# Performance work log

Measured on AMD Instinct MI355X. Metric: run time of the kernel, lower is better.

The kernel has to match this reference:

```python
import jax, jax.numpy as jnp
import numpy as np

C = 1024
HEADS = 8
HEAD_DIM = C // HEADS
SCALE = HEAD_DIM ** -0.5
GROUPS = 32
EPS = 1e-5


def _conv3(x, w, b):
    # 3x3x3 conv, padding=1 (SAME), NCDHW
    y = jax.lax.conv_general_dilated(x, w, (1, 1, 1), 'SAME',
                                     dimension_numbers=('NCDHW', 'OIDHW', 'NCDHW'))
    return y + b[None, :, None, None, None]


def _proj(x, w, b):
    # 1x1x1 conv == channel matmul; w: (C_out, C_in)
    return jnp.einsum('oc,bcdhw->bodhw', w, x) + b[None, :, None, None, None]


def _gn(x, g, b):
    B, Ch, D, H, W = x.shape
    xr = x.reshape(B, GROUPS, Ch // GROUPS, D, H, W)
    mu = xr.mean(axis=(2, 3, 4, 5), keepdims=True)
    var = xr.var(axis=(2, 3, 4, 5), keepdims=True)
    xn = ((xr - mu) * jax.lax.rsqrt(var + EPS)).reshape(B, Ch, D, H, W)
    return xn * g[None, :, None, None, None] + b[None, :, None, None, None]


def _attn(q, k, v):
    # q,k,v: (B,C,D,H,W) -> heads over channels, tokens over flattened spatial
    B, Ch, D, H, W = q.shape
    S = D * H * W
    q = q.reshape(B, HEADS, HEAD_DIM, S)
    k = k.reshape(B, HEADS, HEAD_DIM, S)
    v = v.reshape(B, HEADS, HEAD_DIM, S)
    logits = jnp.einsum('bhds,bhdt->bhst', q, k) * SCALE  # (B,H,S,S)
    a = jax.nn.softmax(logits, axis=-1)
    o = jnp.einsum('bhst,bhdt->bhds', a, v)
    return o.reshape(B, Ch, D, H, W)


def setup_inputs() -> dict:
    key = jax.random.key(0)
    ks = iter(jax.random.split(key, 40))
    def w(shape, s=0.02):
        return jax.random.normal(next(ks), shape, dtype=jnp.float32) * s
    B, D, H, W = 2, 8, 16, 16
    inp = {'x': jax.random.normal(next(ks), (B, C, D, H, W), dtype=jnp.float32)}
    for side in ('l', 'r'):
        inp[f'conv_{side}_w'] = w((C, C, 3, 3, 3))
        inp[f'conv_{side}_b'] = jnp.zeros((C,), jnp.float32)
        inp[f'gn_{side}_g'] = jnp.ones((C,), jnp.float32)
        inp[f'gn_{side}_b'] = jnp.zeros((C,), jnp.float32)
    for name in ('ql', 'kr', 'vr', 'qr', 'kl', 'vl'):
        inp[f'{name}_w'] = w((C, C))
        inp[f'{name}_b'] = jnp.zeros((C,), jnp.float32)
    inp['fus_w'] = w((C, C))
    inp['fus_b'] = jnp.zeros((C,), jnp.float32)
    inp['gn_f_g'] = jnp.ones((C,), jnp.float32)
    inp['gn_f_b'] = jnp.zeros((C,), jnp.float32)
    return inp


def reference(x, conv_l_w, conv_l_b, gn_l_g, gn_l_b,
              conv_r_w, conv_r_b, gn_r_g, gn_r_b,
              ql_w, ql_b, kr_w, kr_b, vr_w, vr_b,
              qr_w, qr_b, kl_w, kl_b, vl_w, vl_b,
              fus_w, fus_b, gn_f_g, gn_f_b):
    W = x.shape[-1]
    mid = W // 2
    x_left = x[..., :mid]
    x_right = x[..., mid:2 * mid]
    f_l = jax.nn.relu(_gn(_conv3(x_left, conv_l_w, conv_l_b), gn_l_g, gn_l_b))
    f_r = jax.nn.relu(_gn(_conv3(x_right, conv_r_w, conv_r_b), gn_r_g, gn_r_b))
    rf = jnp.flip(f_r, axis=-1)
    # left attends to flipped right
    out_l = _attn(_proj(f_l, ql_w, ql_b), _proj(rf, kr_w, kr_b), _proj(rf, vr_w, vr_b))
    # flipped right attends to left
    out_r = _attn(_proj(rf, qr_w, qr_b), _proj(f_l, kl_w, kl_b), _proj(f_l, vl_w, vl_b))
    asym_map = jnp.abs(f_l - rf).mean(axis=1, keepdims=True)
    out_r = jnp.flip(out_r, axis=-1)
    f_concat = jnp.concatenate([out_l, out_r], axis=-1)  # W even -> no pad needed
    fused = jax.nn.relu(_gn(_proj(f_concat, fus_w, fus_b), gn_f_g, gn_f_b))
    return fused, asym_map
```

## Files before the change

### kernel.cpp

```cpp
#include <hip/hip_runtime.h>
#include <hip/hip_bf16.h>
#include <stdint.h>


using bf16_t = __bf16;
using bf16x4 = __attribute__((ext_vector_type(4))) __bf16;
using bf16x8 = __attribute__((ext_vector_type(8))) __bf16;
using f32x4  = __attribute__((ext_vector_type(4))) float;

typedef const uint32_t __attribute__((address_space(1)))* gas1_t;
typedef uint32_t __attribute__((address_space(3)))* las3_t;

__device__ __forceinline__ f32x4 mfma16(bf16x8 a, bf16x8 b, f32x4 c) {
  return __builtin_amdgcn_mfma_f32_16x16x32_bf16(a, b, c, 0, 0, 0);
}
__device__ __forceinline__ void gload_lds16(const void* g, void* l) {
  __builtin_amdgcn_global_load_lds((gas1_t)g, (las3_t)l, 16, 0, 0);
}

__global__ __launch_bounds__(256) void convw_kernel(
    const float* __restrict__ wl, const float* __restrict__ wr,
    bf16_t* __restrict__ Wb)
{
  const int chunk = blockIdx.x;
  const int co    = blockIdx.y;
  const int side  = blockIdx.z;
  const float* __restrict__ src = (side ? wr : wl) + (size_t)co * 27648 + (size_t)chunk * 6912;
  __shared__ float L[6912];
  __shared__ bf16_t Lb[27][260];
  const int tid = threadIdx.x;
  for (int i = tid; i < 1728; i += 256)
    *(float4*)&L[i << 2] = *(const float4*)&src[i << 2];
  __syncthreads();
  {
    const int ci = tid;
#pragma unroll
    for (int t = 0; t < 27; ++t)
      Lb[t][ci] = (bf16_t)L[ci * 27 + t];
  }
  __syncthreads();
  bf16_t* __restrict__ dst = Wb + (size_t)side * (1024u * 27648u) + (size_t)co * 27648 + (chunk << 8);
  for (int u = tid; u < 864; u += 256) {
    const int t = u >> 5, c8 = (u & 31) << 3;
    const bf16x8 v = *(const bf16x8*)&Lb[t][c8];
    *(bf16x8*)&dst[(t << 10) + c8] = v;
  }
}

__global__ __launch_bounds__(256) void projw_kernel(
    const float* ql, const float* kl, const float* kr, const float* qr,
    const float* vl, const float* vr, const float* fu,
    bf16_t* __restrict__ Wp, float qs)
{
  const int z = blockIdx.y;
  const float* src; float s = 1.f;
  switch (z) {
    case 0: src = ql; s = qs; break;
    case 1: src = kl; break;
    case 2: src = kr; break;
    case 3: src = qr; s = qs; break;
    case 4: src = vl; break;
    case 5: src = vr; break;
    default: src = fu; break;
  }
  const size_t i4 = ((size_t)blockIdx.x * 256 + threadIdx.x) * 4;
  const float4 v = *(const float4*)(src + i4);
  bf16x4 o;
  o[0] = (bf16_t)(v.x * s); o[1] = (bf16_t)(v.y * s);
  o[2] = (bf16_t)(v.z * s); o[3] = (bf16_t)(v.w * s);
  *(bf16x4*)(Wp + (size_t)z * 1048576 + i4) = o;
}

__global__ __launch_bounds__(256) void xp_build_kernel(
    const float* __restrict__ x, bf16_t* __restrict__ Xp)
{
  const int cc0  = blockIdx.x << 6;
  const int d    = blockIdx.y;
  const int sb   = blockIdx.z;
  const int side = sb >> 1, b = sb & 1;
  __shared__ bf16_t Tls[64][132];
  const int tid = threadIdx.x;
#pragma unroll
  for (int j = 0; j < 8; ++j) {
    const int u = tid + (j << 8);
    const int ci = u >> 5, sub = u & 31;
    const int hh = sub >> 1, half = sub & 1;
    const float4 v = *(const float4*)&x[((size_t)((b << 10) + cc0 + ci) * 8 + d) * 256 +
                                        (hh << 4) + (side << 3) + (half << 2)];
    bf16x4 o;
    o[0] = (bf16_t)v.x; o[1] = (bf16_t)v.y; o[2] = (bf16_t)v.z; o[3] = (bf16_t)v.w;
    *(bf16x4*)&Tls[ci][(hh << 3) + (half << 2)] = o;
  }
  __syncthreads();
  bf16_t* __restrict__ dst = Xp + (size_t)side * 3686400 + (size_t)b * 1843200;
#pragma unroll
  for (int j = 0; j < 4; ++j) {
    const int u = tid + (j << 8);
    const int hw = u >> 3, c8 = u & 7;
    const int hh = hw >> 3, ww = hw & 7;
    bf16x8 v;
#pragma unroll
    for (int e = 0; e < 8; ++e) v[e] = Tls[(c8 << 3) + e][hw];
    *(bf16x8*)&dst[(size_t)(((d + 1) * 18 + (hh + 1)) * 10 + (ww + 1)) * 1024 + cc0 + (c8 << 3)] = v;
  }
}

__global__ __launch_bounds__(256, 4) void conv_gemm_kernel(
    const bf16_t* __restrict__ Wb, const bf16_t* __restrict__ Xp,
    bf16_t* __restrict__ Pb)
{
  const int bid = blockIdx.x;
  const int orig = ((bid & 7) << 7) | (bid >> 3);
  const int n     = orig & 15;
  const int m0    = ((orig >> 4) & 7) << 7;
  const int side  = (orig >> 7) & 1;
  const int slice = orig >> 8;
  const int t0 = slice * 7;
  const int t1 = (slice == 3) ? 27 : t0 + 7;
  const int b = n >> 3, d = n & 7;

  const bf16_t* __restrict__ A = Wb + (size_t)side * (1024u * 27648u);
  const bf16_t* __restrict__ X = Xp + (size_t)side * 3686400 + (size_t)b * 1843200;

  __shared__ bf16_t Asm[128 * 64];
  __shared__ bf16_t Bsm[128 * 64];

  const int tid = threadIdx.x;
  const int lane = tid & 63;
  const int wv = tid >> 6;
  const int wm = wv >> 1, wn = wv & 1;
  const int lane15 = lane & 15, lane4 = lane >> 4;
  const int srow0 = (wv << 5) + (lane >> 3);
  const int sc = lane & 7;

  const f32x4 fz = {0.f, 0.f, 0.f, 0.f};
  f32x4 acc[4][4];
#pragma unroll
  for (int i = 0; i < 4; ++i)
#pragma unroll
    for (int j = 0; j < 4; ++j) acc[i][j] = fz;

  for (int t = t0; t < t1; ++t) {
    const int kd = t / 9, kh = (t / 3) % 3, kw = t % 3;
    const int sb0 = ((d + kd) * 18 + kh) * 10 + kw;
    for (int cb = 0; cb < 16; ++cb) {
      const int kofs = (t << 10) + (cb << 6);
#pragma unroll
      for (int i = 0; i < 4; ++i) {
        const int row = srow0 + (i << 3);
        gload_lds16(A + (size_t)(m0 + row) * 27648 + kofs + ((sc ^ (row & 7)) << 3),
                    &Asm[((wv << 2) + i) << 9]);
      }
#pragma unroll
      for (int i = 0; i < 4; ++i) {
        const int row = srow0 + (i << 3);
        const int hh = row >> 3, ww = row & 7;
        gload_lds16(X + (size_t)(sb0 + hh * 10 + ww) * 1024 + (cb << 6) + ((sc ^ (row & 7)) << 3),
                    &Bsm[((wv << 2) + i) << 9]);
      }
      __syncthreads();
#pragma unroll
      for (int ks = 0; ks < 2; ++ks) {
        bf16x8 af[4];
#pragma unroll
        for (int mi = 0; mi < 4; ++mi) {
          const int row = (wm << 6) + (mi << 4) + lane15;
          const int ch = ((ks << 2) + lane4) ^ (row & 7);
          af[mi] = *(const bf16x8*)&Asm[(row << 6) + (ch << 3)];
        }
#pragma unroll
        for (int ni = 0; ni < 4; ++ni) {
          const int row = (wn << 6) + (ni << 4) + lane15;
          const int ch = ((ks << 2) + lane4) ^ (row & 7);
          const bf16x8 bfr = *(const bf16x8*)&Bsm[(row << 6) + (ch << 3)];
#pragma unroll
          for (int mi = 0; mi < 4; ++mi)
            acc[mi][ni] = mfma16(af[mi], bfr, acc[mi][ni]);
        }
      }
      __syncthreads();
    }
  }

  bf16_t* __restrict__ P = Pb + (((size_t)(slice << 1) + side) << 21);
  const int colbase = (b << 10) + (d << 7) + (wn << 6);
#pragma unroll
  for (int mi = 0; mi < 4; ++mi) {
    const int row0 = m0 + (wm << 6) + (mi << 4) + (lane4 << 2);
#pragma unroll
    for (int r = 0; r < 4; ++r) {
#pragma unroll
      for (int ni = 0; ni < 4; ++ni) {
        const int col = colbase + (ni << 4) + lane15;
        P[((size_t)(row0 + r) << 11) + col] = (bf16_t)acc[mi][ni][r];
      }
    }
  }
}

__global__ __launch_bounds__(256) void reduce4_kernel(
    const bf16_t* __restrict__ Pb, const float* __restrict__ bias_l,
    const float* __restrict__ bias_r, bf16_t* __restrict__ out_l, bf16_t* __restrict__ out_r,
    float* __restrict__ pS_lr, float* __restrict__ pQ_lr)
{
  const int id = blockIdx.x * 256 + threadIdx.x;
  const int tid = threadIdx.x;
  const int c8 = id & 255;
  const int co = (id >> 8) & 1023;
  const int side = id >> 18;
  const size_t off = ((size_t)co << 11) + ((size_t)c8 << 3);
  const float bia = (side ? bias_r : bias_l)[co];
  float acc[8];
#pragma unroll
  for (int e = 0; e < 8; ++e) acc[e] = bia;
#pragma unroll
  for (int s = 0; s < 4; ++s) {
    const bf16x8 v = *(const bf16x8*)&Pb[(((size_t)(s << 1) + side) << 21) + off];
#pragma unroll
    for (int e = 0; e < 8; ++e) acc[e] += (float)v[e];
  }
  bf16x8 ov;
#pragma unroll
  for (int e = 0; e < 8; ++e) ov[e] = (bf16_t)acc[e];
  *(bf16x8*)((side ? out_r : out_l) + off) = ov;
  float s = 0.f, q = 0.f;
#pragma unroll
  for (int e = 0; e < 8; ++e) { s += acc[e]; q += acc[e] * acc[e]; }
  __shared__ float sb[8];
  const int lane = tid & 63, wv = tid >> 6;
#pragma unroll
  for (int o = 1; o < 64; o <<= 1) { s += __shfl_xor(s, o, 64); q += __shfl_xor(q, o, 64); }
  if (lane == 0) { sb[wv] = s; sb[4 + wv] = q; }
  __syncthreads();
  if (tid == 0) {
    const int g = (side << 6) + (co >> 5);
    atomicAdd(&pS_lr[g],      sb[0] + sb[1]);
    atomicAdd(&pS_lr[g + 32], sb[2] + sb[3]);
    atomicAdd(&pQ_lr[g],      sb[4] + sb[5]);
    atomicAdd(&pQ_lr[g + 32], sb[6] + sb[7]);
  }
}

__device__ __forceinline__ void gemm_accum(
    const bf16_t* __restrict__ A, int lda,
    const bf16_t* __restrict__ Bt, int ldb,
    int K, f32x4 acc[4][4])
{
  __shared__ bf16_t Asm[128 * 64];
  __shared__ bf16_t Bsm[128 * 64];
  const int tid = threadIdx.x;
  const int lane = tid & 63;
  const int wv = tid >> 6;
  const int wm = wv >> 1, wn = wv & 1;
  const int lane15 = lane & 15, lane4 = lane >> 4;
  const int srow0 = (wv << 5) + (lane >> 3);
  const int sc = lane & 7;

  for (int k0 = 0; k0 < K; k0 += 64) {
#pragma unroll
    for (int i = 0; i < 4; ++i) {
      const int row = srow0 + (i << 3);
      gload_lds16(A + (size_t)row * lda + k0 + ((sc ^ (row & 7)) << 3),
                  &Asm[((wv << 2) + i) << 9]);
    }
#pragma unroll
    for (int i = 0; i < 4; ++i) {
      const int row = srow0 + (i << 3);
      gload_lds16(Bt + (size_t)row * ldb + k0 + ((sc ^ (row & 7)) << 3),
                  &Bsm[((wv << 2) + i) << 9]);
    }
    __syncthreads();
#pragma unroll
    for (int ks = 0; ks < 2; ++ks) {
      bf16x8 af[4];
#pragma unroll
      for (int mi = 0; mi < 4; ++mi) {
        const int row = (wm << 6) + (mi << 4) + lane15;
        const int ch = ((ks << 2) + lane4) ^ (row & 7);
        af[mi] = *(const bf16x8*)&Asm[(row << 6) + (ch << 3)];
      }
#pragma unroll
      for (int ni = 0; ni < 4; ++ni) {
        const int row = (wn << 6) + (ni << 4) + lane15;
        const int ch = ((ks << 2) + lane4) ^ (row & 7);
        const bf16x8 bfr = *(const bf16x8*)&Bsm[(row << 6) + (ch << 3)];
#pragma unroll
        for (int mi = 0; mi < 4; ++mi)
          acc[mi][ni] = mfma16(af[mi], bfr, acc[mi][ni]);
      }
    }
    __syncthreads();
  }
}

struct ProjTArgs {
  const bf16_t* act[2];
  const float*  bias[2][2];
  float         scl[2][2];
  bf16_t*       outp[2][2];
};
__global__ __launch_bounds__(256) void proj_t_kernel(const bf16_t* __restrict__ Wp, ProjTArgs a)
{
  const int side = blockIdx.z;
  const int n0 = blockIdx.x << 7;
  const int m0 = blockIdx.y << 7;
  const int seg = m0 >> 10;
  const f32x4 fz = {0.f, 0.f, 0.f, 0.f};
  f32x4 acc[4][4];
#pragma unroll
  for (int i = 0; i < 4; ++i)
#pragma unroll
    for (int j = 0; j < 4; ++j) acc[i][j] = fz;
  gemm_accum(a.act[side] + (size_t)n0 * 1024, 1024,
             Wp + (size_t)side * 2097152 + (size_t)m0 * 1024, 1024, 1024, acc);

  const int lane = threadIdx.x & 63, wv = threadIdx.x >> 6;
  const int wm = wv >> 1, wn = wv & 1;
  const int lane15 = lane & 15, lane4 = lane >> 4;
  const float* __restrict__ bias = a.bias[side][seg];
  const float bscale = a.scl[side][seg];
  bf16_t* __restrict__ C = a.outp[side][seg];
  const int mloc = (m0 & 1023) + (wn << 6);
  float bv[4];
#pragma unroll
  for (int ni = 0; ni < 4; ++ni) bv[ni] = bias[mloc + (ni << 4) + lane15] * bscale;
#pragma unroll
  for (int mi = 0; mi < 4; ++mi) {
    const int rowb = n0 + (wm << 6) + (mi << 4) + (lane4 << 2);
#pragma unroll
    for (int r = 0; r < 4; ++r) {
#pragma unroll
      for (int ni = 0; ni < 4; ++ni) {
        const int col = mloc + (ni << 4) + lane15;
        C[(size_t)(rowb + r) * 1024 + col] = (bf16_t)(acc[mi][ni][r] + bv[ni]);
      }
    }
  }
}

__global__ __launch_bounds__(256) void proj_v_kernel(
    const bf16_t* __restrict__ Wp, const bf16_t* __restrict__ flT,
    const bf16_t* __restrict__ rfT, const float* __restrict__ vlb,
    const float* __restrict__ vrb, bf16_t* __restrict__ Vl, bf16_t* __restrict__ Vr)
{
  const int side = blockIdx.z;
  const int m0 = blockIdx.x << 7;
  const int n0 = blockIdx.y << 7;
  const f32x4 fz = {0.f, 0.f, 0.f, 0.f};
  f32x4 acc[4][4];
#pragma unroll
  for (int i = 0; i < 4; ++i)
#pragma unroll
    for (int j = 0; j < 4; ++j) acc[i][j] = fz;
  gemm_accum(Wp + 4194304ull + (size_t)side * 1048576 + (size_t)m0 * 1024, 1024,
             (side ? rfT : flT) + (size_t)n0 * 1024, 1024, 1024, acc);

  const int lane = threadIdx.x & 63, wv = threadIdx.x >> 6;
  const int wm = wv >> 1, wn = wv & 1;
  const int lane15 = lane & 15, lane4 = lane >> 4;
  const float* __restrict__ bias = side ? vrb : vlb;
  bf16_t* __restrict__ C = side ? Vr : Vl;
#pragma unroll
  for (int mi = 0; mi < 4; ++mi) {
    const int row0 = m0 + (wm << 6) + (mi << 4) + (lane4 << 2);
#pragma unroll
    for (int r = 0; r < 4; ++r) {
      const float bia = bias[row0 + r];
#pragma unroll
      for (int ni = 0; ni < 4; ++ni) {
        const int col = n0 + (wn << 6) + (ni << 4) + lane15;
        C[(size_t)(row0 + r) * 2048 + col] = (bf16_t)(acc[mi][ni][r] + bia);
      }
    }
  }
}

__global__ __launch_bounds__(256) void fused_gemm_kernel(
    const bf16_t* __restrict__ Wf, const bf16_t* __restrict__ Bt, bf16_t* __restrict__ Pf)
{
  const int z = blockIdx.z;
  const int m0 = blockIdx.x << 7;
  const int n0 = blockIdx.y << 7;
  const f32x4 fz = {0.f, 0.f, 0.f, 0.f};
  f32x4 acc[4][4];
#pragma unroll
  for (int i = 0; i < 4; ++i)
#pragma unroll
    for (int j = 0; j < 4; ++j) acc[i][j] = fz;
  gemm_accum(Wf + (size_t)m0 * 1024 + (z << 9), 1024,
             Bt + (size_t)n0 * 1024 + (z << 9), 1024, 512, acc);

  const int lane = threadIdx.x & 63, wv = threadIdx.x >> 6;
  const int wm = wv >> 1, wn = wv & 1;
  const int lane15 = lane & 15, lane4 = lane >> 4;
  bf16_t* __restrict__ C = Pf + ((size_t)z << 22);
#pragma unroll
  for (int mi = 0; mi < 4; ++mi) {
    const int row0 = m0 + (wm << 6) + (mi << 4) + (lane4 << 2);
#pragma unroll
    for (int r = 0; r < 4; ++r) {
#pragma unroll
      for (int ni = 0; ni < 4; ++ni) {
        const int col = n0 + (wn << 6) + (ni << 4) + lane15;
        C[(size_t)(row0 + r) * 4096 + col] = (bf16_t)acc[mi][ni][r];
      }
    }
  }
}

__global__ __launch_bounds__(256) void gn_apply_lr_kernel(
    const bf16_t* __restrict__ yl, const bf16_t* __restrict__ yr,
    const float* __restrict__ gl, const float* __restrict__ bl,
    const float* __restrict__ gr, const float* __restrict__ br,
    const float* __restrict__ pS_lr, const float* __restrict__ pQ_lr,
    bf16_t* __restrict__ flT, bf16_t* __restrict__ rfT)
{
  const int side = blockIdx.z;
  const int n0 = blockIdx.x << 6;
  const int c0 = blockIdx.y << 6;
  const bf16_t* __restrict__ y = side ? yr : yl;
  const float* __restrict__ gamma = side ? gr : gl;
  const float* __restrict__ beta  = side ? br : bl;
  __shared__ float L[64][65];
  const int tid = threadIdx.x;
#pragma unroll
  for (int j = 0; j < 2; ++j) {
    const int u = tid + (j << 8);
    const int cr = u >> 3, ch = u & 7;
    const bf16x8 v = *(const bf16x8*)&y[(size_t)(c0 + cr) * 2048 + n0 + (ch << 3)];
#pragma unroll
    for (int e = 0; e < 8; ++e) L[cr][(ch << 3) + e] = (float)v[e];
  }
  __syncthreads();
  const int b = n0 >> 10;
  bf16_t* __restrict__ outT = side ? rfT : flT;
#pragma unroll
  for (int j = 0; j < 2; ++j) {
    const int u = tid + (j << 8);
    const int nr = u >> 3, c8 = u & 7;
    const int n = n0 + nr;
    const int nf = side ? ((n & ~7) | (7 - (n & 7))) : n;
    const int cbase = c0 + (c8 << 3);
    const int gidx = (side << 6) + (b << 5) + (cbase >> 5);
    const float m = pS_lr[gidx] * (1.f / 32768.f);
    const float rs = rsqrtf(pQ_lr[gidx] * (1.f / 32768.f) - m * m + 1e-5f);
    bf16x8 v;
#pragma unroll
    for (int e = 0; e < 8; ++e) {
      const int c = cbase + e;
      const float xv = (L[(c8 << 3) + e][nr] - m) * rs * gamma[c] + beta[c];
      v[e] = (bf16_t)fmaxf(xv, 0.f);
    }
    *(bf16x8*)&outT[(size_t)nf * 1024 + cbase] = v;
  }
}

__global__ __launch_bounds__(256, 2) void attn_kernel(
    const bf16_t* __restrict__ qlt, const bf16_t* __restrict__ krt, const bf16_t* __restrict__ vrm,
    const bf16_t* __restrict__ qrt, const bf16_t* __restrict__ klt, const bf16_t* __restrict__ vlm,
    bf16_t* __restrict__ xfc)
{
  const int st = blockIdx.x;
  const int bh = blockIdx.y;
  const int az = blockIdx.z;
  const int b = bh >> 3, h = bh & 7;
  const bf16_t* __restrict__ qt = az ? qrt : qlt;
  const bf16_t* __restrict__ kt = az ? klt : krt;
  const bf16_t* __restrict__ vm = az ? vlm : vrm;

  __shared__ bf16_t Ks[64 * 128];
  __shared__ bf16_t Vs[128 * 64];
  __shared__ bf16_t Ps[4][16 * 64];

  const int tid = threadIdx.x, lane = tid & 63, wv = tid >> 6;
  const int lane15 = lane & 15, lane4 = lane >> 4;

  bf16x8 qf[4];
  {
    const bf16_t* __restrict__ qbase = qt + (size_t)((b << 10) + (st << 6)) * 1024 + (h << 7);
    const int row = (wv << 4) + lane15;
#pragma unroll
    for (int kk = 0; kk < 4; ++kk)
      qf[kk] = *(const bf16x8*)&qbase[(size_t)row * 1024 + (kk << 5) + (lane4 << 3)];
  }

  const f32x4 fz = {0.f, 0.f, 0.f, 0.f};
  f32x4 oacc[8];
#pragma unroll
  for (int nj = 0; nj < 8; ++nj) oacc[nj] = fz;
  float mrun[4], lrun[4];
#pragma unroll
  for (int r = 0; r < 4; ++r) { mrun[r] = -3.0e38f; lrun[r] = 0.f; }

  for (int it = 0; it < 16; ++it) {
    __syncthreads();
#pragma unroll
    for (int j = 0; j < 4; ++j) {
      const int g = (wv << 2) + j;
      const int row = (g << 2) + lane4;
      gload_lds16(kt + (size_t)((b << 10) + (it << 6) + row) * 1024 + (h << 7) + ((lane15 ^ (row & 7)) << 3),
                  &Ks[g << 9]);
    }
#pragma unroll
    for (int j = 0; j < 4; ++j) {
      const int g = (wv << 2) + j;
      const int row = (g << 3) + (lane >> 3);
      gload_lds16(vm + (size_t)((h << 7) + row) * 2048 + (b << 10) + (it << 6) + (((lane & 7) ^ (row & 7)) << 3),
                  &Vs[g << 9]);
    }
    __syncthreads();
    f32x4 la[4];
#pragma unroll
    for (int tj = 0; tj < 4; ++tj) la[tj] = fz;
#pragma unroll
    for (int kk = 0; kk < 4; ++kk) {
#pragma unroll
      for (int tj = 0; tj < 4; ++tj) {
        const int row = (tj << 4) + lane15;
        const int ch = ((kk << 2) + lane4) ^ (row & 7);
        const bf16x8 kf = *(const bf16x8*)&Ks[(row << 7) + (ch << 3)];
        la[tj] = mfma16(qf[kk], kf, la[tj]);
      }
    }
    float mx[4];
    int ok = 1;
#pragma unroll
    for (int r = 0; r < 4; ++r) {
      float m_ = la[0][r];
#pragma unroll
      for (int tj = 1; tj < 4; ++tj) m_ = fmaxf(m_, la[tj][r]);
#pragma unroll
      for (int o = 1; o < 16; o <<= 1) m_ = fmaxf(m_, __shfl_xor(m_, o, 64));
      mx[r] = m_;
      ok &= (m_ <= mrun[r] + 8.f) ? 1 : 0;
    }
    if (!__all(ok)) {
#pragma unroll
      for (int r = 0; r < 4; ++r) {
        const float mnew = fmaxf(mrun[r], mx[r]);
        const float alpha = __builtin_amdgcn_exp2f(mrun[r] - mnew);
        mrun[r] = mnew;
        lrun[r] *= alpha;
#pragma unroll
        for (int nj = 0; nj < 8; ++nj) oacc[nj][r] *= alpha;
      }
    }
#pragma unroll
    for (int r = 0; r < 4; ++r) {
      const int row = (lane4 << 2) + r;
      float rs = 0.f;
#pragma unroll
      for (int tj = 0; tj < 4; ++tj) {
        const float p = __builtin_amdgcn_exp2f(la[tj][r] - mrun[r]);
        rs += p;
        const int byte_ = ((tj << 5) + (lane15 << 1)) ^ ((row & 7) << 4);
        *(bf16_t*)((char*)(&Ps[wv][0]) + (row << 7) + byte_) = (bf16_t)p;
      }
#pragma unroll
      for (int o = 1; o < 16; o <<= 1) rs += __shfl_xor(rs, o, 64);
      lrun[r] += rs;
    }
#pragma unroll
    for (int kk = 0; kk < 2; ++kk) {
      const int prow = lane15;
      const int pch = ((kk << 2) + lane4) ^ (prow & 7);
      const bf16x8 pf = *(const bf16x8*)&Ps[wv][(prow << 6) + (pch << 3)];
#pragma unroll
      for (int nj = 0; nj < 8; ++nj) {
        const int row = (nj << 4) + lane15;
        const int ch = ((kk << 2) + lane4) ^ (row & 7);
        const bf16x8 vf = *(const bf16x8*)&Vs[(row << 6) + (ch << 3)];
        oacc[nj] = mfma16(pf, vf, oacc[nj]);
      }
    }
  }
#pragma unroll
  for (int r = 0; r < 4; ++r) {
    const int sl = (wv << 4) + (lane4 << 2) + r;
    const int s = (st << 6) + sl;
    const int dd = s >> 7, hh2 = (s >> 3) & 15, ww = s & 7;
    const int w16 = az ? (15 - ww) : ww;
    const int n16 = (b << 11) + ((dd << 4) + hh2) * 16 + w16;
    const float inv = 1.f / lrun[r];
#pragma unroll
    for (int nj = 0; nj < 8; ++nj) {
      const int c = (h << 7) + (nj << 4) + lane15;
      xfc[(size_t)n16 * 1024 + c] = (bf16_t)(oacc[nj][r] * inv);
    }
  }
}

__global__ __launch_bounds__(256) void gn_partial_f_kernel(
    const bf16_t* __restrict__ Pf, const float* __restrict__ bias,
    float* __restrict__ pS, float* __restrict__ pQ)
{
  const int bg = blockIdx.x;
  const int sl = blockIdx.y;
  const int b = bg >> 5, g = bg & 31;
  const int tid = threadIdx.x;
  const int c = (g << 5) + (tid >> 3);
  const int s0 = (sl << 8) + ((tid & 7) << 5);
  const size_t base = (size_t)c * 4096 + (b << 11) + s0;
  const float bia = bias[c];
  float s = 0.f, q = 0.f;
#pragma unroll
  for (int u = 0; u < 4; ++u) {
    const bf16x8 v0 = *(const bf16x8*)&Pf[base + (u << 3)];
    const bf16x8 v1 = *(const bf16x8*)&Pf[base + (u << 3) + 4194304];
#pragma unroll
    for (int e = 0; e < 8; ++e) {
      const float v = (float)v0[e] + (float)v1[e] + bia;
      s += v; q += v * v;
    }
  }
  __shared__ float sb[8];
  const int lane = tid & 63, wv = tid >> 6;
#pragma unroll
  for (int o = 1; o < 64; o <<= 1) { s += __shfl_xor(s, o, 64); q += __shfl_xor(q, o, 64); }
  if (lane == 0) { sb[wv] = s; sb[4 + wv] = q; }
  __syncthreads();
  if (tid == 0) {
    pS[(bg << 3) + sl] = sb[0] + sb[1] + sb[2] + sb[3];
    pQ[(bg << 3) + sl] = sb[4] + sb[5] + sb[6] + sb[7];
  }
}

__global__ __launch_bounds__(256) void gn_apply_f_kernel(
    const bf16_t* __restrict__ Pf, const float* __restrict__ bias,
    const float* __restrict__ gamma, const float* __restrict__ beta,
    const float* __restrict__ pS, const float* __restrict__ pQ,
    float* __restrict__ outp)
{
  const int id = blockIdx.x * 256 + threadIdx.x;
  const int s8 = id & 255;
  const int c = (id >> 8) & 1023;
  const int b = id >> 18;
  const int gidx = (b << 5) + (c >> 5);
  float S = 0.f, Q = 0.f;
#pragma unroll
  for (int sl = 0; sl < 8; ++sl) { S += pS[(gidx << 3) + sl]; Q += pQ[(gidx << 3) + sl]; }
  const float m = S * (1.f / 65536.f);
  const float rs = rsqrtf(Q * (1.f / 65536.f) - m * m + 1e-5f);
  const float gm = gamma[c], bt = beta[c], bia = bias[c];
  const size_t idx = (size_t)c * 4096 + (b << 11) + (s8 << 3);
  const bf16x8 v0 = *(const bf16x8*)&Pf[idx];
  const bf16x8 v1 = *(const bf16x8*)&Pf[idx + 4194304];
  float o[8];
#pragma unroll
  for (int e = 0; e < 8; ++e) {
    const float v = (float)v0[e] + (float)v1[e] + bia;
    o[e] = fmaxf((v - m) * rs * gm + bt, 0.f);
  }
  float* __restrict__ op = &outp[(((size_t)(b << 10) + c) << 11) + (s8 << 3)];
  float4 o0, o1;
  o0.x = o[0]; o0.y = o[1]; o0.z = o[2]; o0.w = o[3];
  o1.x = o[4]; o1.y = o[5]; o1.z = o[6]; o1.w = o[7];
  *(float4*)op = o0;
  *(float4*)(op + 4) = o1;
}

__global__ __launch_bounds__(256) void asym_kernel(
    const bf16_t* __restrict__ flT, const bf16_t* __restrict__ rfT, float* __restrict__ outp)
{
  const int n = blockIdx.x;
  const int tid = threadIdx.x;
  const bf16x4 a = *(const bf16x4*)&flT[(size_t)n * 1024 + (tid << 2)];
  const bf16x4 c = *(const bf16x4*)&rfT[(size_t)n * 1024 + (tid << 2)];
  float s = 0.f;
#pragma unroll
  for (int e = 0; e < 4; ++e) s += fabsf((float)a[e] - (float)c[e]);
  __shared__ float sb[4];
  const int lane = tid & 63, wv = tid >> 6;
#pragma unroll
  for (int o = 1; o < 64; o <<= 1) s += __shfl_xor(s, o, 64);
  if (lane == 0) sb[wv] = s;
  __syncthreads();
  if (tid == 0) outp[n] = (sb[0] + sb[1] + sb[2] + sb[3]) * (1.f / 1024.f);
}

extern "C" void kernel_launch(void* const* d_in, const int* in_sizes, int n_in,
                              void* d_out, int out_size, void* d_ws, size_t ws_size,
                              hipStream_t stream)
{
  (void)in_sizes; (void)n_in; (void)out_size; (void)ws_size;
  const float* x    = (const float*)d_in[0];
  const float* clw  = (const float*)d_in[1];
  const float* clb  = (const float*)d_in[2];
  const float* glg  = (const float*)d_in[3];
  const float* glb_ = (const float*)d_in[4];
  const float* crw  = (const float*)d_in[5];
  const float* crb  = (const float*)d_in[6];
  const float* grg  = (const float*)d_in[7];
  const float* grb  = (const float*)d_in[8];
  const float* qlw = (const float*)d_in[9];  const float* qlb = (const float*)d_in[10];
  const float* krw = (const float*)d_in[11]; const float* krb = (const float*)d_in[12];
  const float* vrw = (const float*)d_in[13]; const float* vrb = (const float*)d_in[14];
  const float* qrw = (const float*)d_in[15]; const float* qrb = (const float*)d_in[16];
  const float* klw = (const float*)d_in[17]; const float* klb = (const float*)d_in[18];
  const float* vlw = (const float*)d_in[19]; const float* vlb = (const float*)d_in[20];
  const float* fuw = (const float*)d_in[21]; const float* fub = (const float*)d_in[22];
  const float* gfg = (const float*)d_in[23]; const float* gfb = (const float*)d_in[24];
  float* out = (float*)d_out;

  char* ws = (char*)d_ws;
  size_t off = 0;
  auto take = [&](size_t bytes) -> char* {
    char* p = ws + off; off += (bytes + 255) & ~(size_t)255; return p;
  };
  bf16_t* Wb    = (bf16_t*)take(113246208ull);
  bf16_t* Wp    = (bf16_t*)take(14680064ull);
  bf16_t* Xp    = (bf16_t*)take(14745600ull);
  float*  pS_lr = (float*) take(512);
  float*  pQ_lr = (float*) take(512);
  bf16_t* convL = (bf16_t*)take(4194304ull);
  bf16_t* convR = (bf16_t*)take(4194304ull);
  bf16_t* flT   = (bf16_t*)take(4194304ull);
  bf16_t* rfT   = (bf16_t*)take(4194304ull);
  float*  pS    = (float*) take(2048);
  float*  pQ    = (float*) take(2048);
  bf16_t* Pb    = (bf16_t*)take(33554432ull);

  char* al = (char*)Wb; size_t aoff = 0;
  auto takeA = [&](size_t bytes) -> char* {
    char* p = al + aoff; aoff += (bytes + 255) & ~(size_t)255; return p;
  };
  bf16_t* qlT = (bf16_t*)takeA(4194304ull);
  bf16_t* klT = (bf16_t*)takeA(4194304ull);
  bf16_t* krT = (bf16_t*)takeA(4194304ull);
  bf16_t* qrT = (bf16_t*)takeA(4194304ull);
  bf16_t* Vl  = (bf16_t*)takeA(4194304ull);
  bf16_t* Vr  = (bf16_t*)takeA(4194304ull);
  bf16_t* xfcT = (bf16_t*)takeA(8388608ull);
  bf16_t* Pf   = (bf16_t*)takeA(16777216ull);

  const float QS = 0.08838834764831843f * 1.4426950408889634f;

  hipMemsetAsync(Xp, 0, 14745600ull + 1024ull, stream);
  convw_kernel<<<dim3(4, 1024, 2), 256, 0, stream>>>(clw, crw, Wb);
  projw_kernel<<<dim3(1024, 7), 256, 0, stream>>>(qlw, klw, krw, qrw, vlw, vrw, fuw, Wp, QS);
  xp_build_kernel<<<dim3(16, 8, 4), 256, 0, stream>>>(x, Xp);
  conv_gemm_kernel<<<dim3(1024), 256, 0, stream>>>(Wb, Xp, Pb);
  reduce4_kernel<<<dim3(2048), 256, 0, stream>>>(Pb, clb, crb, convL, convR, pS_lr, pQ_lr);
  gn_apply_lr_kernel<<<dim3(32, 16, 2), 256, 0, stream>>>(convL, convR, glg, glb_, grg, grb,
                                                          pS_lr, pQ_lr, flT, rfT);
  ProjTArgs pa;
  pa.act[0] = flT; pa.act[1] = rfT;
  pa.bias[0][0] = qlb; pa.bias[0][1] = klb;
  pa.bias[1][0] = krb; pa.bias[1][1] = qrb;
  pa.scl[0][0] = QS;  pa.scl[0][1] = 1.f;
  pa.scl[1][0] = 1.f; pa.scl[1][1] = QS;
  pa.outp[0][0] = qlT; pa.outp[0][1] = klT;
  pa.outp[1][0] = krT; pa.outp[1][1] = qrT;
  proj_t_kernel<<<dim3(16, 16, 2), 256, 0, stream>>>(Wp, pa);
  proj_v_kernel<<<dim3(8, 16, 2), 256, 0, stream>>>(Wp, flT, rfT, vlb, vrb, Vl, Vr);

  attn_kernel<<<dim3(16, 16, 2), 256, 0, stream>>>(qlT, krT, Vr, qrT, klT, Vl, xfcT);
  fused_gemm_kernel<<<dim3(8, 32, 2), 256, 0, stream>>>(Wp + 6ull * 1048576, xfcT, Pf);
  gn_partial_f_kernel<<<dim3(64, 8), 256, 0, stream>>>(Pf, fub, pS, pQ);
  gn_apply_f_kernel<<<dim3(2048), 256, 0, stream>>>(Pf, fub, gfg, gfb, pS, pQ, out);
  asym_kernel<<<dim3(2048), 256, 0, stream>>>(flT, rfT, out + 4194304);
}
```

Baseline: 467.7 us.

## Rewrite conv GEMM as 256x256-tile, 8-wave double-buffered LDS pipeline

Replaces the 128x128-tile, 4-wave conv implicit GEMM with a 256x256-tile, 512-thread kernel. Global-to-LDS loads are double-buffered and interleaved with MFMA phases, with fine-grained barriers, vmcnt waits and s_setprio raised around the MFMA blocks. The larger tile is meant to raise arithmetic intensity and hide load latency behind compute. In exchange the grid shrinks to 256 blocks, and register and LDS pressure rise to 128 accumulators per thread and 128KB of LDS.

```diff
diff --git a/kernel.cpp b/kernel.cpp
--- a/kernel.cpp
+++ b/kernel.cpp
@@ -105,94 +105,135 @@
   }
 }
 
-__global__ __launch_bounds__(256, 4) void conv_gemm_kernel(
+#define STAGE_A(BUF, H, TILE)                                                 \
+  { const int koff_ = t0k + (TILE) * 64;                                      \
+    gload_lds16(A + (size_t)arow[H][0] * 27648 + koff_ + swz,                 \
+                &Al[BUF][((H) * 128 + (wv << 4)) << 6]);                      \
+    gload_lds16(A + (size_t)arow[H][1] * 27648 + koff_ + swz,                 \
+                &Al[BUF][(((H) * 128 + (wv << 4)) + 8) << 6]); }
+
+#define STAGE_B(BUF, H, TILE)                                                 \
+  { const int t_ = t0 + ((TILE) >> 4);                                        \
+    const int tofs_ = ((t_ / 9) * 18 + ((t_ / 3) % 3)) * 10 + (t_ % 3);       \
+    const int cb64_ = ((TILE) & 15) << 6;                                     \
+    gload_lds16(X + (size_t)(browbase[H][0] + tofs_) * 1024 + cb64_ + swz,    \
+                &Bl[BUF][((H) * 128 + (wv << 4)) << 6]);                      \
+    gload_lds16(X + (size_t)(browbase[H][1] + tofs_) * 1024 + cb64_ + swz,    \
+                &Bl[BUF][(((H) * 128 + (wv << 4)) + 8) << 6]); }
+
+#define PHASE(BUF, MBASE, KS, RDB, VM, ...)                                   \
+  { bf16x8 af[4];                                                             \
+    _Pragma("unroll")                                                         \
+    for (int m_ = 0; m_ < 4; ++m_) {                                          \
+      const int row_ = (wm << 7) + (((MBASE) + m_) << 4) + lane15;            \
+      const int ch_ = (((KS) << 2) + lane4) ^ (row_ & 7);                     \
+      af[m_] = *(const bf16x8*)&Al[BUF][(row_ << 6) + (ch_ << 3)];            \
+    }                                                                         \
+    if (RDB) {                                                                \
+      _Pragma("unroll")                                                       \
+      for (int n_ = 0; n_ < 4; ++n_) {                                        \
+        const int row_ = (wn << 6) + (n_ << 4) + lane15;                      \
+        const int ch_ = (((KS) << 2) + lane4) ^ (row_ & 7);                   \
+        bfr[n_] = *(const bf16x8*)&Bl[BUF][(row_ << 6) + (ch_ << 3)];         \
+      }                                                                       \
+    }                                                                         \
+    __VA_ARGS__;                                                              \
+    __builtin_amdgcn_s_barrier();                                             \
+    asm volatile("s_waitcnt lgkmcnt(0)" ::: "memory");                        \
+    __builtin_amdgcn_s_setprio(1);                                            \
+    _Pragma("unroll")                                                         \
+    for (int m_ = 0; m_ < 4; ++m_)                                            \
+      _Pragma("unroll")                                                       \
+      for (int n_ = 0; n_ < 4; ++n_)                                          \
+        acc[(MBASE) + m_][n_] = mfma16(af[m_], bfr[n_], acc[(MBASE) + m_][n_]);\
+    __builtin_amdgcn_s_setprio(0);                                            \
+    if (VM) asm volatile("s_waitcnt vmcnt(2)" ::: "memory");                  \
+    __builtin_amdgcn_s_barrier(); }
+
+__global__ __launch_bounds__(512, 2) void conv8_kernel(
     const bf16_t* __restrict__ Wb, const bf16_t* __restrict__ Xp,
     bf16_t* __restrict__ Pb)
 {
   const int bid = blockIdx.x;
-  const int orig = ((bid & 7) << 7) | (bid >> 3);
-  const int n     = orig & 15;
-  const int m0    = ((orig >> 4) & 7) << 7;
-  const int side  = (orig >> 7) & 1;
-  const int slice = orig >> 8;
+  const int orig = (bid & 7) * 32 + (bid >> 3);
+  const int ntile = orig & 7;
+  const int mtile = (orig >> 3) & 3;
+  const int side  = (orig >> 5) & 1;
+  const int slice = orig >> 6;
   const int t0 = slice * 7;
-  const int t1 = (slice == 3) ? 27 : t0 + 7;
-  const int b = n >> 3, d = n & 7;
-
-  const bf16_t* __restrict__ A = Wb + (size_t)side * (1024u * 27648u);
+  const int t0k = t0 << 10;
+  const int NTT = (slice == 3) ? 96 : 112;
+  const int n0 = ntile << 8;
+  const int m0 = mtile << 8;
+  const int b = n0 >> 10;
+
+  const bf16_t* __restrict__ A = Wb + (size_t)side * 28311552u;
   const bf16_t* __restrict__ X = Xp + (size_t)side * 3686400 + (size_t)b * 1843200;
 
-  __shared__ bf16_t Asm[128 * 64];
-  __shared__ bf16_t Bsm[128 * 64];
+  __shared__ bf16_t Al[2][256 * 64];
+  __shared__ bf16_t Bl[2][256 * 64];
 
   const int tid = threadIdx.x;
   const int lane = tid & 63;
   const int wv = tid >> 6;
-  const int wm = wv >> 1, wn = wv & 1;
+  const int wm = wv >> 2, wn = wv & 3;
   const int lane15 = lane & 15, lane4 = lane >> 4;
-  const int srow0 = (wv << 5) + (lane >> 3);
-  const int sc = lane & 7;
+  const int l8 = lane >> 3, l7 = lane & 7;
+  const int swz = (l7 ^ l8) << 3;
+
+  int arow[2][2], browbase[2][2];
+#pragma unroll
+  for (int h = 0; h < 2; ++h)
+#pragma unroll
+    for (int j = 0; j < 2; ++j) {
+      const int r = h * 128 + (wv << 4) + (j << 3) + l8;
+      arow[h][j] = m0 + r;
+      const int c = n0 + r;
+      const int d = (c >> 7) & 7, hh = (c >> 3) & 15, ww = c & 7;
+      browbase[h][j] = (d * 18 + hh) * 10 + ww;
+    }
 
   const f32x4 fz = {0.f, 0.f, 0.f, 0.f};
-  f32x4 acc[4][4];
-#pragma unroll
-  for (int i = 0; i < 4; ++i)
+  f32x4 acc[8][4];
+#pragma unroll
+  for (int i = 0; i < 8; ++i)
 #pragma unroll
     for (int j = 0; j < 4; ++j) acc[i][j] = fz;
-
-  for (int t = t0; t < t1; ++t) {
-    const int kd = t / 9, kh = (t / 3) % 3, kw = t % 3;
-    const int sb0 = ((d + kd) * 18 + kh) * 10 + kw;
-    for (int cb = 0; cb < 16; ++cb) {
-      const int kofs = (t << 10) + (cb << 6);
-#pragma unroll
-      for (int i = 0; i < 4; ++i) {
-        const int row = srow0 + (i << 3);
-        gload_lds16(A + (size_t)(m0 + row) * 27648 + kofs + ((sc ^ (row & 7)) << 3),
-                    &Asm[((wv << 2) + i) << 9]);
-      }
-#pragma unroll
-      for (int i = 0; i < 4; ++i) {
-        const int row = srow0 + (i << 3);
-        const int hh = row >> 3, ww = row & 7;
-        gload_lds16(X + (size_t)(sb0 + hh * 10 + ww) * 1024 + (cb << 6) + ((sc ^ (row & 7)) << 3),
-                    &Bsm[((wv << 2) + i) << 9]);
-      }
-      __syncthreads();
-#pragma unroll
-      for (int ks = 0; ks < 2; ++ks) {
-        bf16x8 af[4];
-#pragma unroll
-        for (int mi = 0; mi < 4; ++mi) {
-          const int row = (wm << 6) + (mi << 4) + lane15;
-          const int ch = ((ks << 2) + lane4) ^ (row & 7);
-          af[mi] = *(const bf16x8*)&Asm[(row << 6) + (ch << 3)];
-        }
-#pragma unroll
-        for (int ni = 0; ni < 4; ++ni) {
-          const int row = (wn << 6) + (ni << 4) + lane15;
-          const int ch = ((ks << 2) + lane4) ^ (row & 7);
-          const bf16x8 bfr = *(const bf16x8*)&Bsm[(row << 6) + (ch << 3)];
-#pragma unroll
-          for (int mi = 0; mi < 4; ++mi)
-            acc[mi][ni] = mfma16(af[mi], bfr, acc[mi][ni]);
-        }
-      }
-      __syncthreads();
-    }
+  bf16x8 bfr[4];
+
+  STAGE_B(0, 0, 0)
+  STAGE_B(0, 1, 0)
+  STAGE_A(0, 0, 0)
+  STAGE_A(0, 1, 0)
+  STAGE_B(1, 0, 1)
+  asm volatile("s_waitcnt vmcnt(2)" ::: "memory");
+  __builtin_amdgcn_s_barrier();
+
+  const int NI = NTT >> 1;
+  for (int i = 0; i < NI; ++i) {
+    const int tB = 2 * i + 1;
+    const int tn0 = 2 * i + 2, tn1 = 2 * i + 3;
+    const bool pf = (i + 1 < NI);
+    PHASE(0, 0, 0, true,  false, STAGE_B(1, 1, tB))
+    PHASE(0, 4, 0, false, false, STAGE_A(1, 0, tB))
+    PHASE(0, 0, 1, true,  false, STAGE_A(1, 1, tB))
+    PHASE(0, 4, 1, false, true,  if (pf) STAGE_B(0, 0, tn0))
+    PHASE(1, 0, 0, true,  false, if (pf) STAGE_B(0, 1, tn0))
+    PHASE(1, 4, 0, false, false, if (pf) STAGE_A(0, 0, tn0))
+    PHASE(1, 0, 1, true,  false, if (pf) STAGE_A(0, 1, tn0))
+    PHASE(1, 4, 1, false, true,  if (pf) STAGE_B(1, 0, tn1))
   }
 
   bf16_t* __restrict__ P = Pb + (((size_t)(slice << 1) + side) << 21);
-  const int colbase = (b << 10) + (d << 7) + (wn << 6);
-#pragma unroll
-  for (int mi = 0; mi < 4; ++mi) {
-    const int row0 = m0 + (wm << 6) + (mi << 4) + (lane4 << 2);
+#pragma unroll
+  for (int m = 0; m < 8; ++m) {
+    const int row0 = m0 + (wm << 7) + (m << 4) + (lane4 << 2);
 #pragma unroll
     for (int r = 0; r < 4; ++r) {
 #pragma unroll
-      for (int ni = 0; ni < 4; ++ni) {
-        const int col = colbase + (ni << 4) + lane15;
-        P[((size_t)(row0 + r) << 11) + col] = (bf16_t)acc[mi][ni][r];
+      for (int n = 0; n < 4; ++n) {
+        const int col = n0 + (wn << 6) + (n << 4) + lane15;
+        P[((size_t)(row0 + r) << 11) + col] = (bf16_t)acc[m][n][r];
       }
     }
   }
@@ -739,7 +780,7 @@
   convw_kernel<<<dim3(4, 1024, 2), 256, 0, stream>>>(clw, crw, Wb);
   projw_kernel<<<dim3(1024, 7), 256, 0, stream>>>(qlw, klw, krw, qrw, vlw, vrw, fuw, Wp, QS);
   xp_build_kernel<<<dim3(16, 8, 4), 256, 0, stream>>>(x, Xp);
-  conv_gemm_kernel<<<dim3(1024), 256, 0, stream>>>(Wb, Xp, Pb);
+  conv8_kernel<<<dim3(256), 512, 0, stream>>>(Wb, Xp, Pb);
   reduce4_kernel<<<dim3(2048), 256, 0, stream>>>(Pb, clb, crb, convL, convR, pS_lr, pQ_lr);
   gn_apply_lr_kernel<<<dim3(32, 16, 2), 256, 0, stream>>>(convL, convR, glg, glb_, grg, grb,
                                                           pS_lr, pQ_lr, flT, rfT);
```

Measured after the change: 504.8 us. 7.9% more time.
